# Kernel tuning notes

Hardware: AMD Instinct MI355X
Metric: run time of the kernel (lower is better)

The kernel has to match this reference:

```python
import jax, jax.numpy as jnp
import numpy as np

# Constants matching the module's forward-time configuration
NUM_STAGES = 2
HIDDEN_LENGTH = (512, 1024)   # per-stage video token lengths; S = sum = 1536
ENC_LEN = 128                 # text/encoder token length per sample
B, H, D = 8, 16, 64           # batch (interleaved over stages), heads, head_dim
SEQLENS = (np.array([640, 480, 560, 400], np.int32),     # valid lens, stage 0 (Lc=640)
           np.array([1152, 864, 1008, 720], np.int32))   # valid lens, stage 1 (Lc=1152)


def _pack_indices(seqlens, lc):
    return np.concatenate([i * lc + np.arange(l) for i, l in enumerate(seqlens)]).astype(np.int32)


def setup_inputs() -> dict:
    key = jax.random.key(0)
    ks = jax.random.split(key, 6)
    S = sum(HIDDEN_LENGTH)
    inp = {
        'query':         jax.random.normal(ks[0], (B, S, H, D), jnp.float32),
        'key':           jax.random.normal(ks[1], (B, S, H, D), jnp.float32),
        'value':         jax.random.normal(ks[2], (B, S, H, D), jnp.float32),
        'encoder_query': jax.random.normal(ks[3], (B, ENC_LEN, H, D), jnp.float32),
        'encoder_key':   jax.random.normal(ks[4], (B, ENC_LEN, H, D), jnp.float32),
        'encoder_value': jax.random.normal(ks[5], (B, ENC_LEN, H, D), jnp.float32),
        'indices_0': jnp.asarray(_pack_indices(SEQLENS[0], ENC_LEN + HIDDEN_LENGTH[0])),
        'indices_1': jnp.asarray(_pack_indices(SEQLENS[1], ENC_LEN + HIDDEN_LENGTH[1])),
        'seqlens_0': jnp.asarray(SEQLENS[0]),
        'seqlens_1': jnp.asarray(SEQLENS[1]),
        'heads': 16,
        'scale': jnp.asarray(0.125, jnp.float32),  # 1/sqrt(D)
    }
    return inp


def reference(query, key, value, encoder_query, encoder_key, encoder_value,
              indices_0, indices_1, seqlens_0, seqlens_1, heads, scale):
    # Per stage: take the interleaved batch slice, prepend encoder tokens,
    # run non-causal varlen attention (padded + key-masked == flash_attn_varlen),
    # then gather the valid (packed) rows — faithful to index_first_axis packing.
    indices = (indices_0, indices_1)
    seqlens = (seqlens_0, seqlens_1)
    neg = jnp.finfo(query.dtype).min
    outs = []
    i_sum = 0
    for idx, L in enumerate(HIDDEN_LENGTH):
        q_s = jnp.concatenate([encoder_query[idx::NUM_STAGES], query[idx::NUM_STAGES, i_sum:i_sum + L]], axis=1)
        k_s = jnp.concatenate([encoder_key[idx::NUM_STAGES],   key[idx::NUM_STAGES,   i_sum:i_sum + L]], axis=1)
        v_s = jnp.concatenate([encoder_value[idx::NUM_STAGES], value[idx::NUM_STAGES, i_sum:i_sum + L]], axis=1)
        lc = q_s.shape[1]                                    # enc_len + L
        kmask = jnp.arange(lc)[None, :] < seqlens[idx][:, None]   # [b, lc] key validity
        scores = jnp.einsum('bqhd,bkhd->bhqk', q_s, k_s) * scale  # [b,h,lc,lc]
        scores = jnp.where(kmask[:, None, None, :], scores, neg)
        attn = jax.nn.softmax(scores, axis=-1)
        o = jnp.einsum('bhqk,bkhd->bqhd', attn, v_s)              # [b,lc,h,d]
        o_flat = o.reshape(-1, o.shape[2], o.shape[3])            # [(b*lc),h,d]
        outs.append(o_flat[indices[idx]])                          # pack valid rows
        i_sum += L
    return jnp.concatenate(outs, axis=0)  # [total_packed_tokens, H, D]
```

## Files before the change

### kernel.cpp

```cpp
#include <hip/hip_runtime.h>
#include <hip/hip_bf16.h>

typedef __attribute__((ext_vector_type(8))) __bf16 bf16x8;
typedef __attribute__((ext_vector_type(8))) short short8;
typedef __attribute__((ext_vector_type(4))) float f32x4;
typedef __attribute__((ext_vector_type(4))) unsigned int uint4v;
typedef __attribute__((ext_vector_type(2))) unsigned int uint2v;

#define KS 72
#define LOG2E 1.44269504088896340736f

__device__ __forceinline__ unsigned pack2bf(float lo, float hi) {
    unsigned a = __builtin_bit_cast(unsigned, lo) + 0x8000u;
    unsigned b = __builtin_bit_cast(unsigned, hi) + 0x8000u;
    return __builtin_amdgcn_perm(b, a, 0x07060302u);
}

__device__ __forceinline__ bf16x8 ldfrag(const short* p) {
    short8 s = *reinterpret_cast<const short8*>(p);
    return __builtin_bit_cast(bf16x8, s);
}

__global__ __launch_bounds__(512, 6) void vfa_kernel(
    const float* __restrict__ qv, const float* __restrict__ kv, const float* __restrict__ vv,
    const float* __restrict__ eq, const float* __restrict__ ek, const float* __restrict__ ev,
    const float* __restrict__ scale_p, float* __restrict__ out)
{
    constexpr int H = 16, Dh = 64, ENC = 128, SV = 1536;
    constexpr int SS_CUM[9] = {0,144,272,384,480,560,640,704,768};
    constexpr int SEQL[8] = {1152,1008,864,720,640,560,480,400};
    constexpr int QTN[8]  = {9,8,7,6,5,5,4,4};
    constexpr int OB[8]   = {2080,4096,3232,5104,0,1120,640,1680};
    constexpr int BB[8]   = {1,5,3,7,0,4,2,6};
    constexpr int ISUM[8] = {512,512,512,512,0,0,0,0};

    __shared__ __align__(16) short smem[4*64*KS];

    const int bid = blockIdx.x;
    int ss = 0;
    #pragma unroll
    for (int i = 1; i < 8; ++i) ss += (bid >= SS_CUM[i]) ? 1 : 0;
    const int seqlen   = SEQL[ss];
    const int nqt      = QTN[ss];
    const int b        = BB[ss];
    const int isum     = ISUM[ss];
    const int out_base = OB[ss];
    const int local    = bid - SS_CUM[ss];
    const int head     = local / nqt;
    const int qt       = local - head * nqt;

    const int tid  = threadIdx.x;
    const int wave = tid >> 6;
    const int lane = tid & 63;
    const int quad = lane >> 4;
    const int l15  = lane & 15;

    const float qmul = scale_p[0] * LOG2E;

    const int qrow = qt*128 + wave*16 + l15;
    const float* qrp;
    if (qrow < ENC) qrp = eq + ((b*ENC + qrow)*H + head)*Dh;
    else            qrp = qv + (((b*SV + isum) + (qrow - ENC))*H + head)*Dh;
    bf16x8 qfrag[2];
    #pragma unroll
    for (int f = 0; f < 2; ++f) {
        const float* p = qrp + f*32 + quad*8;
        f32x4 a = *reinterpret_cast<const f32x4*>(p);
        f32x4 c = *reinterpret_cast<const f32x4*>(p + 4);
        uint4v u;
        u[0] = pack2bf(a[0]*qmul, a[1]*qmul);
        u[1] = pack2bf(a[2]*qmul, a[3]*qmul);
        u[2] = pack2bf(c[0]*qmul, c[1]*qmul);
        u[3] = pack2bf(c[2]*qmul, c[3]*qmul);
        qfrag[f] = __builtin_bit_cast(bf16x8, u);
    }

    f32x4 acc[4];
    #pragma unroll
    for (int dt = 0; dt < 4; ++dt) acc[dt] = {0.f,0.f,0.f,0.f};
    float m_s = -INFINITY, l_s = 0.f;

    const int t2  = tid & 255;
    const int klk = t2 >> 2;
    const int kd  = (t2 & 3) * 16;
    const int vk0 = (t2 & 15) * 4;
    const int vd0 = (t2 >> 4) * 4;
    const bool krole = (tid < 256);

    const int nkt = (seqlen + 63) >> 6;
    const int src_base = l15 + ((quad & 1) << 5);

    f32x4 ld0, ld1, ld2, ld3;

    auto issue_loads = [&](int kt_) {
        if (krole) {
            const int kr = kt_*64 + klk;
            const float* krow;
            if (kr < ENC) krow = ek + ((b*ENC + kr)*H + head)*Dh;
            else          krow = kv + (((b*SV + isum) + (kr - ENC))*H + head)*Dh;
            ld0 = *reinterpret_cast<const f32x4*>(krow + kd);
            ld1 = *reinterpret_cast<const f32x4*>(krow + kd + 4);
            ld2 = *reinterpret_cast<const f32x4*>(krow + kd + 8);
            ld3 = *reinterpret_cast<const f32x4*>(krow + kd + 12);
        } else {
            #pragma unroll
            for (int i = 0; i < 4; ++i) {
                const int kr = kt_*64 + vk0 + i;
                const float* vrow;
                if (kr < ENC) vrow = ev + ((b*ENC + kr)*H + head)*Dh;
                else          vrow = vv + (((b*SV + isum) + (kr - ENC))*H + head)*Dh;
                f32x4 t = *reinterpret_cast<const f32x4*>(vrow + vd0);
                if (i == 0) ld0 = t; else if (i == 1) ld1 = t;
                else if (i == 2) ld2 = t; else ld3 = t;
            }
        }
    };

    auto write_tile = [&](short* kb, short* vb) {
        if (krole) {
            uint4v kp;
            kp[0] = pack2bf(ld0[0], ld0[1]);
            kp[1] = pack2bf(ld0[2], ld0[3]);
            kp[2] = pack2bf(ld1[0], ld1[1]);
            kp[3] = pack2bf(ld1[2], ld1[3]);
            *reinterpret_cast<uint4v*>(&kb[klk*KS + kd]) = kp;
            kp[0] = pack2bf(ld2[0], ld2[1]);
            kp[1] = pack2bf(ld2[2], ld2[3]);
            kp[2] = pack2bf(ld3[0], ld3[1]);
            kp[3] = pack2bf(ld3[2], ld3[3]);
            *reinterpret_cast<uint4v*>(&kb[klk*KS + kd + 8]) = kp;
        } else {
            #pragma unroll
            for (int j = 0; j < 4; ++j) {
                uint2v w;
                w[0] = pack2bf(ld0[j], ld1[j]);
                w[1] = pack2bf(ld2[j], ld3[j]);
                *reinterpret_cast<uint2v*>(&vb[(vd0 + j)*KS + vk0]) = w;
            }
        }
    };

    issue_loads(0);

    for (int kt = 0; kt < nkt; ++kt) {
        short* kb = smem + (kt & 1) * (2*64*KS);
        short* vb = kb + 64*KS;

        write_tile(kb, vb);
        if (kt + 1 < nkt) issue_loads(kt + 1);

        asm volatile("s_waitcnt lgkmcnt(0)" ::: "memory");
        __builtin_amdgcn_s_barrier();
        __builtin_amdgcn_sched_barrier(0);

        const int rem  = seqlen - kt*64;
        const int nsub = (rem >= 64) ? 4 : (rem >> 4);

        float s[4][4];
        #pragma unroll
        for (int sub = 0; sub < 4; ++sub) {
            if (sub < nsub) {
                const short* kr0 = &kb[(sub*16 + l15)*KS + quad*8];
                f32x4 sv = {0.f,0.f,0.f,0.f};
                sv = __builtin_amdgcn_mfma_f32_16x16x32_bf16(ldfrag(kr0),      qfrag[0], sv, 0,0,0);
                sv = __builtin_amdgcn_mfma_f32_16x16x32_bf16(ldfrag(kr0 + 32), qfrag[1], sv, 0,0,0);
                #pragma unroll
                for (int r = 0; r < 4; ++r) s[sub][r] = sv[r];
            } else {
                #pragma unroll
                for (int r = 0; r < 4; ++r) s[sub][r] = -INFINITY;
            }
        }

        float mx = s[0][0];
        #pragma unroll
        for (int sub = 0; sub < 4; ++sub)
            #pragma unroll
            for (int r = 0; r < 4; ++r) mx = fmaxf(mx, s[sub][r]);
        mx = fmaxf(mx, __shfl_xor(mx, 16, 64));
        mx = fmaxf(mx, __shfl_xor(mx, 32, 64));
        const float mn = fmaxf(m_s, mx);
        const float alpha = __builtin_amdgcn_exp2f(m_s - mn);
        m_s = mn;
        #pragma unroll
        for (int dt = 0; dt < 4; ++dt)
            #pragma unroll
            for (int r = 0; r < 4; ++r) acc[dt][r] *= alpha;

        float rs = 0.f;
        unsigned pk[4][2];
        #pragma unroll
        for (int sub = 0; sub < 4; ++sub) {
            float p0 = __builtin_amdgcn_exp2f(s[sub][0] - mn);
            float p1 = __builtin_amdgcn_exp2f(s[sub][1] - mn);
            float p2 = __builtin_amdgcn_exp2f(s[sub][2] - mn);
            float p3 = __builtin_amdgcn_exp2f(s[sub][3] - mn);
            rs += (p0 + p1) + (p2 + p3);
            pk[sub][0] = pack2bf(p0, p1);
            pk[sub][1] = pack2bf(p2, p3);
        }
        rs += __shfl_xor(rs, 16, 64);
        rs += __shfl_xor(rs, 32, 64);
        l_s = l_s * alpha + rs;

        #pragma unroll
        for (int kstep = 0; kstep < 2; ++kstep) {
            if (kstep == 0 || nsub > 2) {
                uint4v pf;
                #pragma unroll
                for (int p = 0; p < 4; ++p) {
                    const int sl = src_base + ((p >> 1) << 4);
                    int va = __shfl((int)pk[kstep*2 + 0][p & 1], sl, 64);
                    int vb2 = __shfl((int)pk[kstep*2 + 1][p & 1], sl, 64);
                    pf[p] = (quad & 2) ? (unsigned)vb2 : (unsigned)va;
                }
                bf16x8 pfr = __builtin_bit_cast(bf16x8, pf);
                #pragma unroll
                for (int dt = 0; dt < 4; ++dt) {
                    bf16x8 vfr = ldfrag(&vb[(dt*16 + l15)*KS + kstep*32 + quad*8]);
                    acc[dt] = __builtin_amdgcn_mfma_f32_16x16x32_bf16(vfr, pfr, acc[dt], 0,0,0);
                }
            }
        }
    }

    __syncthreads();
    float* tbuf = reinterpret_cast<float*>(smem);
    const float inv = 1.0f / l_s;
    const int rowl = tid >> 3;
    const int colb = (tid & 7) * 8;
    #pragma unroll
    for (int p = 0; p < 2; ++p) {
        if (p) __syncthreads();
        if ((wave >> 2) == p) {
            #pragma unroll
            for (int dt = 0; dt < 4; ++dt) {
                f32x4 t = acc[dt] * inv;
                *reinterpret_cast<f32x4*>(&tbuf[((wave & 3)*16 + l15)*68 + dt*16 + quad*4]) = t;
            }
        }
        __syncthreads();
        const int grow = qt*128 + p*64 + rowl;
        if (grow < seqlen) {
            float* orow = out + (size_t)(out_base + grow)*(H*Dh) + head*Dh + colb;
            const float* trow = tbuf + rowl*68 + colb;
            *reinterpret_cast<float4*>(orow)     = *reinterpret_cast<const float4*>(trow);
            *reinterpret_cast<float4*>(orow + 4) = *reinterpret_cast<const float4*>(trow + 4);
        }
    }
}

extern "C" void kernel_launch(void* const* d_in, const int* in_sizes, int n_in,
                              void* d_out, int out_size, void* d_ws, size_t ws_size,
                              hipStream_t stream) {
    const float* q     = (const float*)d_in[0];
    const float* k     = (const float*)d_in[1];
    const float* v     = (const float*)d_in[2];
    const float* eq    = (const float*)d_in[3];
    const float* ek    = (const float*)d_in[4];
    const float* ev    = (const float*)d_in[5];
    const float* scale = (const float*)d_in[11];
    float* out = (float*)d_out;

    vfa_kernel<<<dim3(768), dim3(512), 0, stream>>>(q, k, v, eq, ek, ev, scale, out);
}
```

Before: 206.9 us.

## Specialize full KV tiles, lazily rescale softmax, skip inactive query waves

The K/V loading now uses precomputed encoder and video base pointers that advance by a tile stride, replacing per-row address selection on every load. The main loop splits into a fast path for full 64-key tiles and a masked path used only for the last partial tile. The fast path rescales the accumulator only when the running max grows by more than a threshold (wave ballot), and raises wave priority around the MFMA blocks. Waves whose query rows lie beyond seqlen skip compute entirely. These remove branch and exp/multiply overhead, and the lazy rescale carries a small risk of fp32 overflow margin in exchange.

```diff
diff --git a/kernel.cpp b/kernel.cpp
--- a/kernel.cpp
+++ b/kernel.cpp
@@ -27,6 +27,8 @@
     const float* __restrict__ scale_p, float* __restrict__ out)
 {
     constexpr int H = 16, Dh = 64, ENC = 128, SV = 1536;
+    constexpr int ROWF = H*Dh;
+    constexpr int TILEF = 64*ROWF;
     constexpr int SS_CUM[9] = {0,144,272,384,480,560,640,704,768};
     constexpr int SEQL[8] = {1152,1008,864,720,640,560,480,400};
     constexpr int QTN[8]  = {9,8,7,6,5,5,4,4};
@@ -87,33 +89,23 @@
     const int vd0 = (t2 >> 4) * 4;
     const bool krole = (tid < 256);
 
-    const int nkt = (seqlen + 63) >> 6;
-    const int src_base = l15 + ((quad & 1) << 5);
+    const float* encP = krole
+        ? ek + ((size_t)(b*ENC + klk)*H + head)*Dh + kd
+        : ev + ((size_t)(b*ENC + vk0)*H + head)*Dh + vd0;
+    const float* vidP = krole
+        ? kv + ((size_t)((b*SV + isum) + klk)*H + head)*Dh + kd
+        : vv + ((size_t)((b*SV + isum) + vk0)*H + head)*Dh + vd0;
+    const int o1 = krole ? 4 : ROWF;
+    const int o2 = krole ? 8 : 2*ROWF;
+    const int o3 = krole ? 12 : 3*ROWF;
 
     f32x4 ld0, ld1, ld2, ld3;
 
-    auto issue_loads = [&](int kt_) {
-        if (krole) {
-            const int kr = kt_*64 + klk;
-            const float* krow;
-            if (kr < ENC) krow = ek + ((b*ENC + kr)*H + head)*Dh;
-            else          krow = kv + (((b*SV + isum) + (kr - ENC))*H + head)*Dh;
-            ld0 = *reinterpret_cast<const f32x4*>(krow + kd);
-            ld1 = *reinterpret_cast<const f32x4*>(krow + kd + 4);
-            ld2 = *reinterpret_cast<const f32x4*>(krow + kd + 8);
-            ld3 = *reinterpret_cast<const f32x4*>(krow + kd + 12);
-        } else {
-            #pragma unroll
-            for (int i = 0; i < 4; ++i) {
-                const int kr = kt_*64 + vk0 + i;
-                const float* vrow;
-                if (kr < ENC) vrow = ev + ((b*ENC + kr)*H + head)*Dh;
-                else          vrow = vv + (((b*SV + isum) + (kr - ENC))*H + head)*Dh;
-                f32x4 t = *reinterpret_cast<const f32x4*>(vrow + vd0);
-                if (i == 0) ld0 = t; else if (i == 1) ld1 = t;
-                else if (i == 2) ld2 = t; else ld3 = t;
-            }
-        }
+    auto issue = [&](const float* base) {
+        ld0 = *reinterpret_cast<const f32x4*>(base);
+        ld1 = *reinterpret_cast<const f32x4*>(base + o1);
+        ld2 = *reinterpret_cast<const f32x4*>(base + o2);
+        ld3 = *reinterpret_cast<const f32x4*>(base + o3);
     };
 
     auto write_tile = [&](short* kb, short* vb) {
@@ -140,38 +132,96 @@
         }
     };
 
-    issue_loads(0);
-
-    for (int kt = 0; kt < nkt; ++kt) {
-        short* kb = smem + (kt & 1) * (2*64*KS);
-        short* vb = kb + 64*KS;
-
-        write_tile(kb, vb);
-        if (kt + 1 < nkt) issue_loads(kt + 1);
-
-        asm volatile("s_waitcnt lgkmcnt(0)" ::: "memory");
-        __builtin_amdgcn_s_barrier();
-        __builtin_amdgcn_sched_barrier(0);
-
-        const int rem  = seqlen - kt*64;
-        const int nsub = (rem >= 64) ? 4 : (rem >> 4);
-
+    const int nkt = (seqlen + 63) >> 6;
+    const int nsub_last = ((seqlen & 63) ? ((seqlen & 63) >> 4) : 4);
+    const int nfull = (nsub_last == 4) ? nkt : nkt - 1;
+    const bool active_q = (qt*128 + wave*16) < seqlen;
+    const int src_base = l15 + ((quad & 1) << 5);
+
+    auto compute_full = [&](const short* kb, const short* vb) {
+        f32x4 sv[4];
+        __builtin_amdgcn_s_setprio(1);
+        #pragma unroll
+        for (int sub = 0; sub < 4; ++sub) {
+            const short* kr0 = &kb[(sub*16 + l15)*KS + quad*8];
+            f32x4 t = {0.f,0.f,0.f,0.f};
+            t = __builtin_amdgcn_mfma_f32_16x16x32_bf16(ldfrag(kr0),      qfrag[0], t, 0,0,0);
+            t = __builtin_amdgcn_mfma_f32_16x16x32_bf16(ldfrag(kr0 + 32), qfrag[1], t, 0,0,0);
+            sv[sub] = t;
+        }
+        __builtin_amdgcn_s_setprio(0);
+
+        float m0 = fmaxf(fmaxf(sv[0][0], sv[0][1]), fmaxf(sv[0][2], sv[0][3]));
+        float m1 = fmaxf(fmaxf(sv[1][0], sv[1][1]), fmaxf(sv[1][2], sv[1][3]));
+        float m2 = fmaxf(fmaxf(sv[2][0], sv[2][1]), fmaxf(sv[2][2], sv[2][3]));
+        float m3 = fmaxf(fmaxf(sv[3][0], sv[3][1]), fmaxf(sv[3][2], sv[3][3]));
+        float mx = fmaxf(fmaxf(m0, m1), fmaxf(m2, m3));
+        mx = fmaxf(mx, __shfl_xor(mx, 16, 64));
+        mx = fmaxf(mx, __shfl_xor(mx, 32, 64));
+
+        if (__ballot(mx > m_s + 8.f)) {
+            const float mn = fmaxf(m_s, mx);
+            const float alpha = __builtin_amdgcn_exp2f(m_s - mn);
+            #pragma unroll
+            for (int dt = 0; dt < 4; ++dt) acc[dt] *= alpha;
+            l_s *= alpha;
+            m_s = mn;
+        }
+
+        float rs = 0.f;
+        unsigned pk[4][2];
+        #pragma unroll
+        for (int sub = 0; sub < 4; ++sub) {
+            float p0 = __builtin_amdgcn_exp2f(sv[sub][0] - m_s);
+            float p1 = __builtin_amdgcn_exp2f(sv[sub][1] - m_s);
+            float p2 = __builtin_amdgcn_exp2f(sv[sub][2] - m_s);
+            float p3 = __builtin_amdgcn_exp2f(sv[sub][3] - m_s);
+            rs += (p0 + p1) + (p2 + p3);
+            pk[sub][0] = pack2bf(p0, p1);
+            pk[sub][1] = pack2bf(p2, p3);
+        }
+        rs += __shfl_xor(rs, 16, 64);
+        rs += __shfl_xor(rs, 32, 64);
+        l_s += rs;
+
+        #pragma unroll
+        for (int kstep = 0; kstep < 2; ++kstep) {
+            uint4v pf;
+            #pragma unroll
+            for (int p = 0; p < 4; ++p) {
+                const int sl = src_base + ((p >> 1) << 4);
+                int va = __shfl((int)pk[kstep*2 + 0][p & 1], sl, 64);
+                int vb2 = __shfl((int)pk[kstep*2 + 1][p & 1], sl, 64);
+                pf[p] = (quad & 2) ? (unsigned)vb2 : (unsigned)va;
+            }
+            bf16x8 pfr = __builtin_bit_cast(bf16x8, pf);
+            __builtin_amdgcn_s_setprio(1);
+            #pragma unroll
+            for (int dt = 0; dt < 4; ++dt) {
+                bf16x8 vfr = ldfrag(&vb[(dt*16 + l15)*KS + kstep*32 + quad*8]);
+                acc[dt] = __builtin_amdgcn_mfma_f32_16x16x32_bf16(vfr, pfr, acc[dt], 0,0,0);
+            }
+            __builtin_amdgcn_s_setprio(0);
+        }
+    };
+
+    auto compute_partial = [&](const short* kb, const short* vb) {
+        const int nsub = nsub_last;
         float s[4][4];
         #pragma unroll
         for (int sub = 0; sub < 4; ++sub) {
             if (sub < nsub) {
                 const short* kr0 = &kb[(sub*16 + l15)*KS + quad*8];
-                f32x4 sv = {0.f,0.f,0.f,0.f};
-                sv = __builtin_amdgcn_mfma_f32_16x16x32_bf16(ldfrag(kr0),      qfrag[0], sv, 0,0,0);
-                sv = __builtin_amdgcn_mfma_f32_16x16x32_bf16(ldfrag(kr0 + 32), qfrag[1], sv, 0,0,0);
+                f32x4 t = {0.f,0.f,0.f,0.f};
+                t = __builtin_amdgcn_mfma_f32_16x16x32_bf16(ldfrag(kr0),      qfrag[0], t, 0,0,0);
+                t = __builtin_amdgcn_mfma_f32_16x16x32_bf16(ldfrag(kr0 + 32), qfrag[1], t, 0,0,0);
                 #pragma unroll
-                for (int r = 0; r < 4; ++r) s[sub][r] = sv[r];
+                for (int r = 0; r < 4; ++r) s[sub][r] = t[r];
             } else {
                 #pragma unroll
                 for (int r = 0; r < 4; ++r) s[sub][r] = -INFINITY;
             }
         }
-
         float mx = s[0][0];
         #pragma unroll
         for (int sub = 0; sub < 4; ++sub)
@@ -183,9 +233,7 @@
         const float alpha = __builtin_amdgcn_exp2f(m_s - mn);
         m_s = mn;
         #pragma unroll
-        for (int dt = 0; dt < 4; ++dt)
-            #pragma unroll
-            for (int r = 0; r < 4; ++r) acc[dt][r] *= alpha;
+        for (int dt = 0; dt < 4; ++dt) acc[dt] *= alpha;
 
         float rs = 0.f;
         unsigned pk[4][2];
@@ -222,6 +270,28 @@
                 }
             }
         }
+    };
+
+    issue(encP);
+    for (int t = 0; t < nkt; ++t) {
+        short* kb = smem + (t & 1) * (2*64*KS);
+        short* vb = kb + 64*KS;
+
+        write_tile(kb, vb);
+        const int nx = t + 1;
+        if (nx < nkt) {
+            if (nx == 1) issue(encP + TILEF);
+            else { issue(vidP); vidP += TILEF; }
+        }
+
+        asm volatile("s_waitcnt lgkmcnt(0)" ::: "memory");
+        __builtin_amdgcn_s_barrier();
+        __builtin_amdgcn_sched_barrier(0);
+
+        if (active_q) {
+            if (t < nfull) compute_full(kb, vb);
+            else           compute_partial(kb, vb);
+        }
     }
 
     __syncthreads();
```

Result: slower. 272.4 us (+31.7%).

## Use lazy softmax rescaling, skip inactive query waves, and simplify K/V address math

Applied to the files above, without the earlier changes.

The K/V load addressing is simplified to precomputed base pointers with fixed strides, since ENC=128 makes tile 0 and tile 1 encoder rows and later tiles video rows. Waves whose query rows are all beyond seqlen skip the compute while still taking part in loads and barriers. The online-softmax rescale becomes conditional, applied only when some lane's max grows by more than 8 in log2 units, which trades a bounded growth of exponent values for fewer rescales. s_setprio is raised around the MFMA sections to favour matrix issue across waves.

```diff
diff --git a/kernel.cpp b/kernel.cpp
--- a/kernel.cpp
+++ b/kernel.cpp
@@ -27,6 +27,8 @@
     const float* __restrict__ scale_p, float* __restrict__ out)
 {
     constexpr int H = 16, Dh = 64, ENC = 128, SV = 1536;
+    constexpr int ROWF = H*Dh;
+    constexpr int TILEF = 64*ROWF;
     constexpr int SS_CUM[9] = {0,144,272,384,480,560,640,704,768};
     constexpr int SEQL[8] = {1152,1008,864,720,640,560,480,400};
     constexpr int QTN[8]  = {9,8,7,6,5,5,4,4};
@@ -87,32 +89,29 @@
     const int vd0 = (t2 >> 4) * 4;
     const bool krole = (tid < 256);
 
-    const int nkt = (seqlen + 63) >> 6;
-    const int src_base = l15 + ((quad & 1) << 5);
+    const float* encP;
+    const float* vidP;
+    if (krole) {
+        encP = ek + ((size_t)(b*ENC + klk)*H + head)*Dh + kd;
+        vidP = kv + ((size_t)((b*SV + isum) + klk)*H + head)*Dh + kd;
+    } else {
+        encP = ev + ((size_t)(b*ENC + vk0)*H + head)*Dh + vd0;
+        vidP = vv + ((size_t)((b*SV + isum) + vk0)*H + head)*Dh + vd0;
+    }
 
     f32x4 ld0, ld1, ld2, ld3;
 
-    auto issue_loads = [&](int kt_) {
+    auto issue = [&](const float* base) {
         if (krole) {
-            const int kr = kt_*64 + klk;
-            const float* krow;
-            if (kr < ENC) krow = ek + ((b*ENC + kr)*H + head)*Dh;
-            else          krow = kv + (((b*SV + isum) + (kr - ENC))*H + head)*Dh;
-            ld0 = *reinterpret_cast<const f32x4*>(krow + kd);
-            ld1 = *reinterpret_cast<const f32x4*>(krow + kd + 4);
-            ld2 = *reinterpret_cast<const f32x4*>(krow + kd + 8);
-            ld3 = *reinterpret_cast<const f32x4*>(krow + kd + 12);
+            ld0 = *reinterpret_cast<const f32x4*>(base);
+            ld1 = *reinterpret_cast<const f32x4*>(base + 4);
+            ld2 = *reinterpret_cast<const f32x4*>(base + 8);
+            ld3 = *reinterpret_cast<const f32x4*>(base + 12);
         } else {
-            #pragma unroll
-            for (int i = 0; i < 4; ++i) {
-                const int kr = kt_*64 + vk0 + i;
-                const float* vrow;
-                if (kr < ENC) vrow = ev + ((b*ENC + kr)*H + head)*Dh;
-                else          vrow = vv + (((b*SV + isum) + (kr - ENC))*H + head)*Dh;
-                f32x4 t = *reinterpret_cast<const f32x4*>(vrow + vd0);
-                if (i == 0) ld0 = t; else if (i == 1) ld1 = t;
-                else if (i == 2) ld2 = t; else ld3 = t;
-            }
+            ld0 = *reinterpret_cast<const f32x4*>(base);
+            ld1 = *reinterpret_cast<const f32x4*>(base + ROWF);
+            ld2 = *reinterpret_cast<const f32x4*>(base + 2*ROWF);
+            ld3 = *reinterpret_cast<const f32x4*>(base + 3*ROWF);
         }
     };
 
@@ -140,23 +139,34 @@
         }
     };
 
-    issue_loads(0);
+    const int nkt = (seqlen + 63) >> 6;
+    const bool active_q = (qt*128 + wave*16) < seqlen;
+    const int src_base = l15 + ((quad & 1) << 5);
+
+    issue(encP);
 
     for (int kt = 0; kt < nkt; ++kt) {
         short* kb = smem + (kt & 1) * (2*64*KS);
         short* vb = kb + 64*KS;
 
         write_tile(kb, vb);
-        if (kt + 1 < nkt) issue_loads(kt + 1);
+        const int nx = kt + 1;
+        if (nx < nkt) {
+            if (nx == 1) issue(encP + TILEF);
+            else { issue(vidP); vidP += TILEF; }
+        }
 
         asm volatile("s_waitcnt lgkmcnt(0)" ::: "memory");
         __builtin_amdgcn_s_barrier();
         __builtin_amdgcn_sched_barrier(0);
 
+        if (!active_q) continue;
+
         const int rem  = seqlen - kt*64;
         const int nsub = (rem >= 64) ? 4 : (rem >> 4);
 
         float s[4][4];
+        __builtin_amdgcn_s_setprio(1);
         #pragma unroll
         for (int sub = 0; sub < 4; ++sub) {
             if (sub < nsub) {
@@ -171,6 +181,7 @@
                 for (int r = 0; r < 4; ++r) s[sub][r] = -INFINITY;
             }
         }
+        __builtin_amdgcn_s_setprio(0);
 
         float mx = s[0][0];
         #pragma unroll
@@ -179,29 +190,31 @@
             for (int r = 0; r < 4; ++r) mx = fmaxf(mx, s[sub][r]);
         mx = fmaxf(mx, __shfl_xor(mx, 16, 64));
         mx = fmaxf(mx, __shfl_xor(mx, 32, 64));
-        const float mn = fmaxf(m_s, mx);
-        const float alpha = __builtin_amdgcn_exp2f(m_s - mn);
-        m_s = mn;
-        #pragma unroll
-        for (int dt = 0; dt < 4; ++dt)
-            #pragma unroll
-            for (int r = 0; r < 4; ++r) acc[dt][r] *= alpha;
+
+        if (__ballot(mx > m_s + 8.f)) {
+            const float mn = fmaxf(m_s, mx);
+            const float alpha = __builtin_amdgcn_exp2f(m_s - mn);
+            #pragma unroll
+            for (int dt = 0; dt < 4; ++dt) acc[dt] *= alpha;
+            l_s *= alpha;
+            m_s = mn;
+        }
 
         float rs = 0.f;
         unsigned pk[4][2];
         #pragma unroll
         for (int sub = 0; sub < 4; ++sub) {
-            float p0 = __builtin_amdgcn_exp2f(s[sub][0] - mn);
-            float p1 = __builtin_amdgcn_exp2f(s[sub][1] - mn);
-            float p2 = __builtin_amdgcn_exp2f(s[sub][2] - mn);
-            float p3 = __builtin_amdgcn_exp2f(s[sub][3] - mn);
+            float p0 = __builtin_amdgcn_exp2f(s[sub][0] - m_s);
+            float p1 = __builtin_amdgcn_exp2f(s[sub][1] - m_s);
+            float p2 = __builtin_amdgcn_exp2f(s[sub][2] - m_s);
+            float p3 = __builtin_amdgcn_exp2f(s[sub][3] - m_s);
             rs += (p0 + p1) + (p2 + p3);
             pk[sub][0] = pack2bf(p0, p1);
             pk[sub][1] = pack2bf(p2, p3);
         }
         rs += __shfl_xor(rs, 16, 64);
         rs += __shfl_xor(rs, 32, 64);
-        l_s = l_s * alpha + rs;
+        l_s += rs;
 
         #pragma unroll
         for (int kstep = 0; kstep < 2; ++kstep) {
@@ -215,11 +228,13 @@
                     pf[p] = (quad & 2) ? (unsigned)vb2 : (unsigned)va;
                 }
                 bf16x8 pfr = __builtin_bit_cast(bf16x8, pf);
+                __builtin_amdgcn_s_setprio(1);
                 #pragma unroll
                 for (int dt = 0; dt < 4; ++dt) {
                     bf16x8 vfr = ldfrag(&vb[(dt*16 + l15)*KS + kstep*32 + quad*8]);
                     acc[dt] = __builtin_amdgcn_mfma_f32_16x16x32_bf16(vfr, pfr, acc[dt], 0,0,0);
                 }
+                __builtin_amdgcn_s_setprio(0);
             }
         }
     }
```

Result: slower. 215.4 us (+4.1%).

## Split waves into producer K/V loaders and consumers computing two query groups

Applied to the files above, without the earlier changes.

Dedicates four waves to loading and bf16-converting K and V tiles into shared memory, while the other four waves each process two 16-row query groups, reusing each K fragment across both groups. This removes the per-wave load/compute interleaving and the register prefetch of the next tile, and aims to reduce LDS K-fragment reads per query row. The loads are now issued in the same iteration right before the barrier, so global latency is no longer hidden behind the previous tile's compute. Half the waves do no MFMA work. Launch bounds are relaxed to allow more registers.

```diff
diff --git a/kernel.cpp b/kernel.cpp
--- a/kernel.cpp
+++ b/kernel.cpp
@@ -21,12 +21,13 @@
     return __builtin_bit_cast(bf16x8, s);
 }
 
-__global__ __launch_bounds__(512, 6) void vfa_kernel(
+__global__ __launch_bounds__(512, 4) void vfa_kernel(
     const float* __restrict__ qv, const float* __restrict__ kv, const float* __restrict__ vv,
     const float* __restrict__ eq, const float* __restrict__ ek, const float* __restrict__ ev,
     const float* __restrict__ scale_p, float* __restrict__ out)
 {
     constexpr int H = 16, Dh = 64, ENC = 128, SV = 1536;
+    constexpr int ROWF = H*Dh;
     constexpr int SS_CUM[9] = {0,144,272,384,480,560,640,704,768};
     constexpr int SEQL[8] = {1152,1008,864,720,640,560,480,400};
     constexpr int QTN[8]  = {9,8,7,6,5,5,4,4};
@@ -54,171 +55,182 @@
     const int lane = tid & 63;
     const int quad = lane >> 4;
     const int l15  = lane & 15;
+    const bool consumer = (wave < 4);
 
     const float qmul = scale_p[0] * LOG2E;
 
-    const int qrow = qt*128 + wave*16 + l15;
-    const float* qrp;
-    if (qrow < ENC) qrp = eq + ((b*ENC + qrow)*H + head)*Dh;
-    else            qrp = qv + (((b*SV + isum) + (qrow - ENC))*H + head)*Dh;
-    bf16x8 qfrag[2];
+    bf16x8 qfrag[2][2];
+    f32x4  acc[2][4];
+    float  m_s[2] = {-INFINITY, -INFINITY};
+    float  l_s[2] = {0.f, 0.f};
     #pragma unroll
-    for (int f = 0; f < 2; ++f) {
-        const float* p = qrp + f*32 + quad*8;
-        f32x4 a = *reinterpret_cast<const f32x4*>(p);
-        f32x4 c = *reinterpret_cast<const f32x4*>(p + 4);
-        uint4v u;
-        u[0] = pack2bf(a[0]*qmul, a[1]*qmul);
-        u[1] = pack2bf(a[2]*qmul, a[3]*qmul);
-        u[2] = pack2bf(c[0]*qmul, c[1]*qmul);
-        u[3] = pack2bf(c[2]*qmul, c[3]*qmul);
-        qfrag[f] = __builtin_bit_cast(bf16x8, u);
+    for (int g = 0; g < 2; ++g)
+        #pragma unroll
+        for (int dt = 0; dt < 4; ++dt) acc[g][dt] = {0.f,0.f,0.f,0.f};
+
+    if (consumer) {
+        #pragma unroll
+        for (int g = 0; g < 2; ++g) {
+            const int qrow = qt*128 + wave*32 + g*16 + l15;
+            const float* qrp;
+            if (qrow < ENC) qrp = eq + ((size_t)(b*ENC + qrow)*H + head)*Dh;
+            else            qrp = qv + ((size_t)((b*SV + isum) + (qrow - ENC))*H + head)*Dh;
+            #pragma unroll
+            for (int f = 0; f < 2; ++f) {
+                const float* p = qrp + f*32 + quad*8;
+                f32x4 a = *reinterpret_cast<const f32x4*>(p);
+                f32x4 c = *reinterpret_cast<const f32x4*>(p + 4);
+                uint4v u;
+                u[0] = pack2bf(a[0]*qmul, a[1]*qmul);
+                u[1] = pack2bf(a[2]*qmul, a[3]*qmul);
+                u[2] = pack2bf(c[0]*qmul, c[1]*qmul);
+                u[3] = pack2bf(c[2]*qmul, c[3]*qmul);
+                qfrag[g][f] = __builtin_bit_cast(bf16x8, u);
+            }
+        }
     }
-
-    f32x4 acc[4];
-    #pragma unroll
-    for (int dt = 0; dt < 4; ++dt) acc[dt] = {0.f,0.f,0.f,0.f};
-    float m_s = -INFINITY, l_s = 0.f;
-
-    const int t2  = tid & 255;
-    const int klk = t2 >> 2;
-    const int kd  = (t2 & 3) * 16;
-    const int vk0 = (t2 & 15) * 4;
-    const int vd0 = (t2 >> 4) * 4;
-    const bool krole = (tid < 256);
 
     const int nkt = (seqlen + 63) >> 6;
     const int src_base = l15 + ((quad & 1) << 5);
-
-    f32x4 ld0, ld1, ld2, ld3;
-
-    auto issue_loads = [&](int kt_) {
-        if (krole) {
-            const int kr = kt_*64 + klk;
-            const float* krow;
-            if (kr < ENC) krow = ek + ((b*ENC + kr)*H + head)*Dh;
-            else          krow = kv + (((b*SV + isum) + (kr - ENC))*H + head)*Dh;
-            ld0 = *reinterpret_cast<const f32x4*>(krow + kd);
-            ld1 = *reinterpret_cast<const f32x4*>(krow + kd + 4);
-            ld2 = *reinterpret_cast<const f32x4*>(krow + kd + 8);
-            ld3 = *reinterpret_cast<const f32x4*>(krow + kd + 12);
-        } else {
-            #pragma unroll
-            for (int i = 0; i < 4; ++i) {
-                const int kr = kt_*64 + vk0 + i;
-                const float* vrow;
-                if (kr < ENC) vrow = ev + ((b*ENC + kr)*H + head)*Dh;
-                else          vrow = vv + (((b*SV + isum) + (kr - ENC))*H + head)*Dh;
-                f32x4 t = *reinterpret_cast<const f32x4*>(vrow + vd0);
-                if (i == 0) ld0 = t; else if (i == 1) ld1 = t;
-                else if (i == 2) ld2 = t; else ld3 = t;
-            }
-        }
-    };
-
-    auto write_tile = [&](short* kb, short* vb) {
-        if (krole) {
-            uint4v kp;
-            kp[0] = pack2bf(ld0[0], ld0[1]);
-            kp[1] = pack2bf(ld0[2], ld0[3]);
-            kp[2] = pack2bf(ld1[0], ld1[1]);
-            kp[3] = pack2bf(ld1[2], ld1[3]);
-            *reinterpret_cast<uint4v*>(&kb[klk*KS + kd]) = kp;
-            kp[0] = pack2bf(ld2[0], ld2[1]);
-            kp[1] = pack2bf(ld2[2], ld2[3]);
-            kp[2] = pack2bf(ld3[0], ld3[1]);
-            kp[3] = pack2bf(ld3[2], ld3[3]);
-            *reinterpret_cast<uint4v*>(&kb[klk*KS + kd + 8]) = kp;
-        } else {
-            #pragma unroll
-            for (int j = 0; j < 4; ++j) {
-                uint2v w;
-                w[0] = pack2bf(ld0[j], ld1[j]);
-                w[1] = pack2bf(ld2[j], ld3[j]);
-                *reinterpret_cast<uint2v*>(&vb[(vd0 + j)*KS + vk0]) = w;
-            }
-        }
-    };
-
-    issue_loads(0);
+    const int pidx = tid & 127;
 
     for (int kt = 0; kt < nkt; ++kt) {
         short* kb = smem + (kt & 1) * (2*64*KS);
         short* vb = kb + 64*KS;
 
-        write_tile(kb, vb);
-        if (kt + 1 < nkt) issue_loads(kt + 1);
-
-        asm volatile("s_waitcnt lgkmcnt(0)" ::: "memory");
+        if (!consumer) {
+            if (wave < 6) {
+                const int prow = pidx & 63;
+                const int pd0  = (pidx >> 6) * 32;
+                const int kr = kt*64 + prow;
+                const float* base = (kr < ENC)
+                    ? ek + ((size_t)(b*ENC + kr)*H + head)*Dh + pd0
+                    : kv + ((size_t)((b*SV + isum) + (kr - ENC))*H + head)*Dh + pd0;
+                f32x4 pl[8];
+                #pragma unroll
+                for (int i = 0; i < 8; ++i)
+                    pl[i] = *reinterpret_cast<const f32x4*>(base + 4*i);
+                short* dst = &kb[prow*KS + pd0];
+                #pragma unroll
+                for (int m = 0; m < 4; ++m) {
+                    uint4v w;
+                    w[0] = pack2bf(pl[2*m][0],   pl[2*m][1]);
+                    w[1] = pack2bf(pl[2*m][2],   pl[2*m][3]);
+                    w[2] = pack2bf(pl[2*m+1][0], pl[2*m+1][1]);
+                    w[3] = pack2bf(pl[2*m+1][2], pl[2*m+1][3]);
+                    *reinterpret_cast<uint4v*>(dst + m*8) = w;
+                }
+            } else {
+                const int pk0 = (pidx & 15) * 4;
+                const int pd0 = (pidx >> 4) * 8;
+                const int kr = kt*64 + pk0;
+                const float* base = (kr < ENC)
+                    ? ev + ((size_t)(b*ENC + kr)*H + head)*Dh + pd0
+                    : vv + ((size_t)((b*SV + isum) + (kr - ENC))*H + head)*Dh + pd0;
+                f32x4 pl[8];
+                #pragma unroll
+                for (int r = 0; r < 4; ++r) {
+                    pl[2*r]   = *reinterpret_cast<const f32x4*>(base + r*ROWF);
+                    pl[2*r+1] = *reinterpret_cast<const f32x4*>(base + r*ROWF + 4);
+                }
+                #pragma unroll
+                for (int j = 0; j < 4; ++j) {
+                    uint2v w;
+                    w[0] = pack2bf(pl[0][j], pl[2][j]);
+                    w[1] = pack2bf(pl[4][j], pl[6][j]);
+                    *reinterpret_cast<uint2v*>(&vb[(pd0 + j)*KS + pk0]) = w;
+                }
+                #pragma unroll
+                for (int j = 0; j < 4; ++j) {
+                    uint2v w;
+                    w[0] = pack2bf(pl[1][j], pl[3][j]);
+                    w[1] = pack2bf(pl[5][j], pl[7][j]);
+                    *reinterpret_cast<uint2v*>(&vb[(pd0 + 4 + j)*KS + pk0]) = w;
+                }
+            }
+            asm volatile("s_waitcnt lgkmcnt(0)" ::: "memory");
+        }
         __builtin_amdgcn_s_barrier();
         __builtin_amdgcn_sched_barrier(0);
 
-        const int rem  = seqlen - kt*64;
-        const int nsub = (rem >= 64) ? 4 : (rem >> 4);
-
-        float s[4][4];
-        #pragma unroll
-        for (int sub = 0; sub < 4; ++sub) {
-            if (sub < nsub) {
-                const short* kr0 = &kb[(sub*16 + l15)*KS + quad*8];
-                f32x4 sv = {0.f,0.f,0.f,0.f};
-                sv = __builtin_amdgcn_mfma_f32_16x16x32_bf16(ldfrag(kr0),      qfrag[0], sv, 0,0,0);
-                sv = __builtin_amdgcn_mfma_f32_16x16x32_bf16(ldfrag(kr0 + 32), qfrag[1], sv, 0,0,0);
-                #pragma unroll
-                for (int r = 0; r < 4; ++r) s[sub][r] = sv[r];
-            } else {
-                #pragma unroll
-                for (int r = 0; r < 4; ++r) s[sub][r] = -INFINITY;
-            }
-        }
-
-        float mx = s[0][0];
-        #pragma unroll
-        for (int sub = 0; sub < 4; ++sub)
-            #pragma unroll
-            for (int r = 0; r < 4; ++r) mx = fmaxf(mx, s[sub][r]);
-        mx = fmaxf(mx, __shfl_xor(mx, 16, 64));
-        mx = fmaxf(mx, __shfl_xor(mx, 32, 64));
-        const float mn = fmaxf(m_s, mx);
-        const float alpha = __builtin_amdgcn_exp2f(m_s - mn);
-        m_s = mn;
-        #pragma unroll
-        for (int dt = 0; dt < 4; ++dt)
-            #pragma unroll
-            for (int r = 0; r < 4; ++r) acc[dt][r] *= alpha;
-
-        float rs = 0.f;
-        unsigned pk[4][2];
-        #pragma unroll
-        for (int sub = 0; sub < 4; ++sub) {
-            float p0 = __builtin_amdgcn_exp2f(s[sub][0] - mn);
-            float p1 = __builtin_amdgcn_exp2f(s[sub][1] - mn);
-            float p2 = __builtin_amdgcn_exp2f(s[sub][2] - mn);
-            float p3 = __builtin_amdgcn_exp2f(s[sub][3] - mn);
-            rs += (p0 + p1) + (p2 + p3);
-            pk[sub][0] = pack2bf(p0, p1);
-            pk[sub][1] = pack2bf(p2, p3);
-        }
-        rs += __shfl_xor(rs, 16, 64);
-        rs += __shfl_xor(rs, 32, 64);
-        l_s = l_s * alpha + rs;
-
-        #pragma unroll
-        for (int kstep = 0; kstep < 2; ++kstep) {
-            if (kstep == 0 || nsub > 2) {
-                uint4v pf;
-                #pragma unroll
-                for (int p = 0; p < 4; ++p) {
-                    const int sl = src_base + ((p >> 1) << 4);
-                    int va = __shfl((int)pk[kstep*2 + 0][p & 1], sl, 64);
-                    int vb2 = __shfl((int)pk[kstep*2 + 1][p & 1], sl, 64);
-                    pf[p] = (quad & 2) ? (unsigned)vb2 : (unsigned)va;
-                }
-                bf16x8 pfr = __builtin_bit_cast(bf16x8, pf);
-                #pragma unroll
-                for (int dt = 0; dt < 4; ++dt) {
-                    bf16x8 vfr = ldfrag(&vb[(dt*16 + l15)*KS + kstep*32 + quad*8]);
-                    acc[dt] = __builtin_amdgcn_mfma_f32_16x16x32_bf16(vfr, pfr, acc[dt], 0,0,0);
+        if (consumer) {
+            const int rem  = seqlen - kt*64;
+            const int nsub = (rem >= 64) ? 4 : (rem >> 4);
+
+            f32x4 sv[2][4];
+            const f32x4 ninf = {-INFINITY,-INFINITY,-INFINITY,-INFINITY};
+            #pragma unroll
+            for (int sub = 0; sub < 4; ++sub) {
+                if (sub < nsub) {
+                    const short* kr0 = &kb[(sub*16 + l15)*KS + quad*8];
+                    bf16x8 kf0 = ldfrag(kr0);
+                    bf16x8 kf1 = ldfrag(kr0 + 32);
+                    #pragma unroll
+                    for (int g = 0; g < 2; ++g) {
+                        f32x4 t = {0.f,0.f,0.f,0.f};
+                        t = __builtin_amdgcn_mfma_f32_16x16x32_bf16(kf0, qfrag[g][0], t, 0,0,0);
+                        t = __builtin_amdgcn_mfma_f32_16x16x32_bf16(kf1, qfrag[g][1], t, 0,0,0);
+                        sv[g][sub] = t;
+                    }
+                } else {
+                    sv[0][sub] = ninf;
+                    sv[1][sub] = ninf;
+                }
+            }
+
+            unsigned pk[2][4][2];
+            #pragma unroll
+            for (int g = 0; g < 2; ++g) {
+                float mx = sv[g][0][0];
+                #pragma unroll
+                for (int sub = 0; sub < 4; ++sub)
+                    #pragma unroll
+                    for (int r = 0; r < 4; ++r) mx = fmaxf(mx, sv[g][sub][r]);
+                mx = fmaxf(mx, __shfl_xor(mx, 16, 64));
+                mx = fmaxf(mx, __shfl_xor(mx, 32, 64));
+                const float mn = fmaxf(m_s[g], mx);
+                const float alpha = __builtin_amdgcn_exp2f(m_s[g] - mn);
+                m_s[g] = mn;
+                #pragma unroll
+                for (int dt = 0; dt < 4; ++dt) acc[g][dt] *= alpha;
+
+                float rs = 0.f;
+                #pragma unroll
+                for (int sub = 0; sub < 4; ++sub) {
+                    float p0 = __builtin_amdgcn_exp2f(sv[g][sub][0] - mn);
+                    float p1 = __builtin_amdgcn_exp2f(sv[g][sub][1] - mn);
+                    float p2 = __builtin_amdgcn_exp2f(sv[g][sub][2] - mn);
+                    float p3 = __builtin_amdgcn_exp2f(sv[g][sub][3] - mn);
+                    rs += (p0 + p1) + (p2 + p3);
+                    pk[g][sub][0] = pack2bf(p0, p1);
+                    pk[g][sub][1] = pack2bf(p2, p3);
+                }
+                rs += __shfl_xor(rs, 16, 64);
+                rs += __shfl_xor(rs, 32, 64);
+                l_s[g] = l_s[g] * alpha + rs;
+            }
+
+            #pragma unroll
+            for (int kstep = 0; kstep < 2; ++kstep) {
+                if (kstep == 0 || nsub > 2) {
+                    uint4v pfv[2];
+                    #pragma unroll
+                    for (int g = 0; g < 2; ++g)
+                        #pragma unroll
+                        for (int p = 0; p < 4; ++p) {
+                            const int sl = src_base + ((p >> 1) << 4);
+                            int va  = __shfl((int)pk[g][kstep*2 + 0][p & 1], sl, 64);
+                            int vb2 = __shfl((int)pk[g][kstep*2 + 1][p & 1], sl, 64);
+                            pfv[g][p] = (quad & 2) ? (unsigned)vb2 : (unsigned)va;
+                        }
+                    bf16x8 pfr0 = __builtin_bit_cast(bf16x8, pfv[0]);
+                    bf16x8 pfr1 = __builtin_bit_cast(bf16x8, pfv[1]);
+                    #pragma unroll
+                    for (int dt = 0; dt < 4; ++dt) {
+                        bf16x8 vfr = ldfrag(&vb[(dt*16 + l15)*KS + kstep*32 + quad*8]);
+                        acc[0][dt] = __builtin_amdgcn_mfma_f32_16x16x32_bf16(vfr, pfr0, acc[0][dt], 0,0,0);
+                        acc[1][dt] = __builtin_amdgcn_mfma_f32_16x16x32_bf16(vfr, pfr1, acc[1][dt], 0,0,0);
+                    }
                 }
             }
         }
@@ -226,17 +238,21 @@
 
     __syncthreads();
     float* tbuf = reinterpret_cast<float*>(smem);
-    const float inv = 1.0f / l_s;
+    const float inv0 = 1.0f / l_s[0];
+    const float inv1 = 1.0f / l_s[1];
     const int rowl = tid >> 3;
     const int colb = (tid & 7) * 8;
     #pragma unroll
     for (int p = 0; p < 2; ++p) {
         if (p) __syncthreads();
-        if ((wave >> 2) == p) {
+        if (consumer && (wave >> 1) == p) {
+            const int rbase = (wave & 1) * 32;
             #pragma unroll
             for (int dt = 0; dt < 4; ++dt) {
-                f32x4 t = acc[dt] * inv;
-                *reinterpret_cast<f32x4*>(&tbuf[((wave & 3)*16 + l15)*68 + dt*16 + quad*4]) = t;
+                f32x4 tA = acc[0][dt] * inv0;
+                f32x4 tB = acc[1][dt] * inv1;
+                *reinterpret_cast<f32x4*>(&tbuf[(rbase + l15)*68      + dt*16 + quad*4]) = tA;
+                *reinterpret_cast<f32x4*>(&tbuf[(rbase + 16 + l15)*68 + dt*16 + quad*4]) = tB;
             }
         }
         __syncthreads();
```

Result: slower. 211.6 us (+2.3%).
